# Optimization experiments

Measured on AMD Instinct MI355X. Metric: run time of the kernel, lower is better.

The kernel has to match this reference:

```python
import jax, jax.numpy as jnp
import numpy as np

B, S, D, H = 2, 2048, 1024, 16
HD = D // H  # head_dim = 64


def setup_inputs() -> dict:
    key = jax.random.key(0)
    ks = jax.random.split(key, 5)
    scale = 0.02
    return {
        "x": jax.random.normal(ks[0], (B, S, D), dtype=jnp.float32),
        "w_qkv": jax.random.normal(ks[1], (D, 3 * D), dtype=jnp.float32) * scale,
        "b_qkv": jax.random.normal(ks[2], (3 * D,), dtype=jnp.float32) * scale,
        "w_out": jax.random.normal(ks[3], (D, D), dtype=jnp.float32) * scale,
        "b_out": jax.random.normal(ks[4], (D,), dtype=jnp.float32) * scale,
    }


def reference(x, w_qkv, b_qkv, w_out, b_out):
    b, s, d = x.shape
    qkv = x @ w_qkv + b_qkv                       # [b,s,3d]
    q, k, v = jnp.split(qkv, 3, axis=-1)
    # split heads -> [b,h,s,hd]
    def split_heads(t):
        return t.reshape(b, s, H, HD).transpose(0, 2, 1, 3)
    q, k, v = split_heads(q), split_heads(k), split_heads(v)
    scores = jnp.einsum('bhqd,bhkd->bhqk', q, k) / jnp.sqrt(jnp.float32(HD))
    causal = jnp.tril(jnp.ones((s, s), dtype=bool))  # [s,s]
    scores = jnp.where(causal[None, None], scores, -jnp.inf)
    attn = jax.nn.softmax(scores, axis=-1)        # dropout_p=0 -> identity
    ctx = jnp.einsum('bhqk,bhkd->bhqd', attn, v)
    ctx = ctx.transpose(0, 2, 1, 3).reshape(b, s, d)  # merge heads
    return ctx @ w_out + b_out
```

## Files before the change

### kernel.cpp

```cpp
#include <hip/hip_runtime.h>
#include <hip/hip_bf16.h>

#define B_ 2
#define S_ 2048
#define D_ 1024
#define H_ 16
#define HD_ 64
#define KDIM 1024
#define QKVW 3072

typedef __attribute__((ext_vector_type(8))) short s16x8;
typedef __attribute__((ext_vector_type(8))) __bf16 bf16x8;
typedef __attribute__((ext_vector_type(4))) float f32x4;
typedef __attribute__((ext_vector_type(16))) float f32x16;
typedef __attribute__((ext_vector_type(4))) unsigned short u16x4;

__device__ __forceinline__ unsigned short f2bf(float f) {
  union { __bf16 b; unsigned short u; } v;
  v.b = (__bf16)f;
  return v.u;
}

__device__ __forceinline__ unsigned pk2(float lo, float hi) {
  union { unsigned short s[2]; unsigned u; } r;
  r.s[0] = f2bf(lo); r.s[1] = f2bf(hi);
  return r.u;
}

__device__ __forceinline__ void plswap2(unsigned& a_out, unsigned& b_out,
                                        unsigned a, unsigned b) {
  auto rr = __builtin_amdgcn_permlane32_swap(a, b, false, false);
  unsigned out[2];
  __builtin_memcpy(out, &rr, 8);
  a_out = out[0];
  b_out = out[1];
}

#define MFMA16(a, b, c) __builtin_amdgcn_mfma_f32_16x16x32_bf16((a), (b), (c), 0, 0, 0)
#define MFMA32(a, b, c) __builtin_amdgcn_mfma_f32_32x32x16_bf16((a), (b), (c), 0, 0, 0)

__device__ __forceinline__ void gll16(const void* g, void* l) {
  __builtin_amdgcn_global_load_lds(
      (const __attribute__((address_space(1))) void*)g,
      (__attribute__((address_space(3))) void*)l, 16, 0, 0);
}

__global__ __launch_bounds__(256) void prep(const float* __restrict__ X,
                                            unsigned short* __restrict__ Xb,
                                            const float* __restrict__ Wq,
                                            unsigned short* __restrict__ WqT,
                                            const float* __restrict__ Wo,
                                            unsigned short* __restrict__ WoT) {
  const int bid = blockIdx.x;
  const int t = threadIdx.x;
  if (bid < 2048) {
    const int i = (bid * 256 + t) * 8;
    const float4 a = *reinterpret_cast<const float4*>(X + i);
    const float4 b = *reinterpret_cast<const float4*>(X + i + 4);
    u16x4 lo = {f2bf(a.x), f2bf(a.y), f2bf(a.z), f2bf(a.w)};
    u16x4 hi = {f2bf(b.x), f2bf(b.y), f2bf(b.z), f2bf(b.w)};
    *reinterpret_cast<u16x4*>(Xb + i) = lo;
    *reinterpret_cast<u16x4*>(Xb + i + 4) = hi;
    return;
  }
  __shared__ float T[64][65];
  const float* W;
  unsigned short* Wt;
  int N, k0, n0;
  if (bid < 2048 + 768) {
    const int i = bid - 2048;
    W = Wq; Wt = WqT; N = 3072;
    n0 = (i % 48) * 64; k0 = (i / 48) * 64;
  } else {
    const int i = bid - 2816;
    W = Wo; Wt = WoT; N = 1024;
    n0 = (i % 16) * 64; k0 = (i / 16) * 64;
  }
  const int lr = t >> 4, lc = (t & 15) * 4;
#pragma unroll
  for (int p = 0; p < 4; ++p) {
    const int r = lr + p * 16;
    const float4 v = *reinterpret_cast<const float4*>(W + (size_t)(k0 + r) * N + n0 + lc);
    T[r][lc + 0] = v.x; T[r][lc + 1] = v.y; T[r][lc + 2] = v.z; T[r][lc + 3] = v.w;
  }
  __syncthreads();
  const int wn = t >> 4, wk = (t & 15) * 4;
#pragma unroll
  for (int p = 0; p < 4; ++p) {
    const int n = wn + p * 16;
    u16x4 o = {f2bf(T[wk + 0][n]), f2bf(T[wk + 1][n]), f2bf(T[wk + 2][n]), f2bf(T[wk + 3][n])};
    *reinterpret_cast<u16x4*>(Wt + (size_t)(n0 + n) * 1024 + k0 + wk) = o;
  }
}

__global__ __launch_bounds__(256) void vtrans(const unsigned short* __restrict__ QKVc,
                                              unsigned short* __restrict__ Vt) {
  __shared__ unsigned short T[64][72];
  const int s0 = blockIdx.x * 64;
  const int bh = blockIdx.y;
  const int bb = bh >> 4, hh = bh & 15;
  const int t = threadIdx.x;
  const size_t base = (size_t)bh * (S_ * HD_);
  const int r = t >> 3, c8 = (t & 7) * 8;
#pragma unroll
  for (int p = 0; p < 2; ++p)
    *reinterpret_cast<s16x8*>(&T[r + p * 32][c8]) =
        *reinterpret_cast<const s16x8*>(
            QKVc + (size_t)(bb * S_ + s0 + r + p * 32) * QKVW + 2048 + hh * 64 + c8);
  __syncthreads();
  const int hd = t & 63, sg = (t >> 6) * 8;
#pragma unroll
  for (int p = 0; p < 2; ++p) {
    unsigned short tmp[8];
#pragma unroll
    for (int j = 0; j < 8; ++j) tmp[j] = T[sg + p * 32 + j][hd];
    *reinterpret_cast<s16x8*>(Vt + base + (size_t)hd * S_ + s0 + sg + p * 32) =
        *reinterpret_cast<s16x8*>(tmp);
  }
}

__global__ __launch_bounds__(256) void gemm_qkv(
    const unsigned short* __restrict__ Xb, const unsigned short* __restrict__ WT,
    const float* __restrict__ bias, unsigned short* __restrict__ Cq) {
  __shared__ __align__(16) unsigned short As[2][64 * 64];
  __shared__ __align__(16) unsigned short Bs[2][128 * 64];
  const int bid = blockIdx.y * 24 + blockIdx.x;
  const int xcd = bid & 7, rr = bid >> 3;
  const int m0 = ((xcd >> 1) * 16 + (rr & 15)) * 64;
  const int n0 = ((xcd & 1) * 12 + (rr >> 4)) * 128;
  const int t = threadIdx.x;
  const int lane = t & 63, wid = t >> 6;
  const int wr = wid >> 1, wc = wid & 1;
  const int l15 = lane & 15, l16 = lane >> 4;
  const int srow = lane >> 3, scol = ((lane & 7) ^ srow) << 3;
  f32x4 acc[2][4] = {};

#define GSTAGE(buf, k0)                                                              \
  do {                                                                               \
    _Pragma("unroll") for (int c = 0; c < 2; ++c) {                                  \
      const int r8 = wid * 16 + c * 8;                                               \
      gll16(Xb + (size_t)(m0 + r8 + srow) * KDIM + (k0) + scol, &As[buf][r8 * 64]);  \
    }                                                                                \
    _Pragma("unroll") for (int c = 0; c < 4; ++c) {                                  \
      const int r8 = wid * 32 + c * 8;                                               \
      gll16(WT + (size_t)(n0 + r8 + srow) * KDIM + (k0) + scol, &Bs[buf][r8 * 64]);  \
    }                                                                                \
  } while (0)

  GSTAGE(0, 0);
  for (int kt = 0; kt < 16; ++kt) {
    const int cur = kt & 1;
    if (kt + 1 < 16) {
      GSTAGE(cur ^ 1, (kt + 1) * 64);
      __asm__ volatile("s_waitcnt vmcnt(6)" ::: "memory");
    } else {
      __asm__ volatile("s_waitcnt vmcnt(0)" ::: "memory");
    }
    __builtin_amdgcn_s_barrier();
    const int key = (l15 & 7) << 4;
    const char* ab = (const char*)&As[cur][0] + (wr * 32 + l15) * 128;
    const char* bb = (const char*)&Bs[cur][0] + (wc * 64 + l15) * 128;
#pragma unroll
    for (int ks = 0; ks < 2; ++ks) {
      bf16x8 af[2], bfr[4];
#pragma unroll
      for (int m = 0; m < 2; ++m)
        af[m] = *(const bf16x8*)(ab + m * 2048 + ((ks * 64 + l16 * 16) ^ key));
#pragma unroll
      for (int n = 0; n < 4; ++n)
        bfr[n] = *(const bf16x8*)(bb + n * 2048 + ((ks * 64 + l16 * 16) ^ key));
#pragma unroll
      for (int m = 0; m < 2; ++m)
#pragma unroll
        for (int n = 0; n < 4; ++n)
          acc[m][n] = MFMA16(af[m], bfr[n], acc[m][n]);
    }
    __builtin_amdgcn_s_barrier();
  }
#pragma unroll
  for (int n = 0; n < 4; ++n) {
    const int col = n0 + wc * 64 + n * 16 + l15;
    const float bv = bias[col];
#pragma unroll
    for (int m = 0; m < 2; ++m) {
#pragma unroll
      for (int j = 0; j < 4; ++j) {
        const int row = m0 + wr * 32 + m * 16 + l16 * 4 + j;
        Cq[(size_t)row * QKVW + col] = f2bf(acc[m][n][j] + bv);
      }
    }
  }
}

__global__ __launch_bounds__(256, 3) void attn(
    const unsigned short* __restrict__ QKVc, const unsigned short* __restrict__ Vt,
    unsigned short* __restrict__ Cxt) {
  __shared__ __align__(16) unsigned short Kl[2][2][4096];
  __shared__ __align__(16) unsigned short Vl[2][4096];
  const int bi = blockIdx.x;
  const int xcd = bi & 7, slot = bi >> 3;
  const int bh = xcd * 4 + (slot & 3);
  const int qt = 31 - (slot >> 2);
  const int t = threadIdx.x, lane = t & 63, wid = t >> 6;
  const int qw = wid & 1, pw = wid >> 1;
  const int l31 = lane & 31, h = lane >> 5;
  const int h8 = h * 8, h16 = h * 16, h4 = h * 4;
  const int bb = bh >> 4, hh = bh & 15;
  const size_t base = (size_t)bh * (S_ * HD_);
  const int q0 = qt * 64 + qw * 32;
  const float NEG = -1e30f;
  const float SCALE = 0.18033688011112042f;
  const float FM = 10.0f;
  const int srow = lane >> 3;
  const int scol = ((lane & 7) ^ srow) << 3;

  bf16x8 qf[4];
  {
    const unsigned short* qp =
        QKVc + (size_t)(bb * S_ + q0 + l31) * QKVW + hh * 64 + h8;
#pragma unroll
    for (int ks = 0; ks < 4; ++ks) qf[ks] = *reinterpret_cast<const bf16x8*>(qp + ks * 16);
  }
  f32x16 o0 = {}, o1 = {};
  float lacc[8] = {};

#define STAGEK(buf, kvb)                                                              \
  do {                                                                                \
    _Pragma("unroll") for (int c = 0; c < 8; ++c)                                     \
      gll16(QKVc + (size_t)(bb * S_ + (kvb) + c * 8 + srow) * QKVW + 1024 +           \
                hh * 64 + scol,                                                       \
            &Kl[buf][pw][c * 8 * 64]);                                                \
  } while (0)

#define STAGEV(kvb)                                                                   \
  do {                                                                                \
    _Pragma("unroll") for (int c = 0; c < 8; ++c)                                     \
      gll16(Vt + base + (size_t)(c * 8 + srow) * S_ + (kvb) + scol,                   \
            &Vl[pw][c * 8 * 64]);                                                     \
  } while (0)

#define COMPUTE_QK(cb, tcur)                                                         \
  do {                                                                               \
    const int kv0 = (tcur) * 64;                                                     \
    const bool diag = (kv0 + 63 > q0);                                               \
    const char* kbase = (const char*)&Kl[cb][pw][0];                                 \
    const int key = (l31 & 7) << 4;                                                  \
    f32x16 s0 = {}, s1 = {};                                                         \
    __builtin_amdgcn_s_setprio(1);                                                   \
    _Pragma("unroll") for (int ks = 0; ks < 4; ++ks) {                               \
      bf16x8 ka = *(const bf16x8*)(kbase + l31 * 128 + ((ks * 32 + h16) ^ key));     \
      s0 = MFMA32(ka, qf[ks], s0);                                                   \
    }                                                                                \
    if (f2) {                                                                        \
      _Pragma("unroll") for (int ks = 0; ks < 4; ++ks) {                             \
        bf16x8 kb = *(const bf16x8*)(kbase + (32 + l31) * 128 + ((ks * 32 + h16) ^ key)); \
        s1 = MFMA32(kb, qf[ks], s1);                                                 \
      }                                                                              \
    }                                                                                \
    __builtin_amdgcn_s_setprio(0);                                                   \
    if (diag) {                                                                      \
      const int lim0 = q0 + l31 - kv0;                                               \
      const int lim1 = lim0 - 32;                                                    \
      _Pragma("unroll") for (int r = 0; r < 16; ++r) {                               \
        const int cr = (r & 3) + 8 * (r >> 2) + h4;                                  \
        if (cr > lim0) s0[r] = NEG;                                                  \
        if (f2 && cr > lim1) s1[r] = NEG;                                            \
      }                                                                              \
    }                                                                                \
    _Pragma("unroll") for (int r = 0; r < 16; ++r)                                   \
      s0[r] = exp2f(fmaf(s0[r], SCALE, -FM));                                        \
    if (f2) {                                                                        \
      _Pragma("unroll") for (int r = 0; r < 16; ++r)                                 \
        s1[r] = exp2f(fmaf(s1[r], SCALE, -FM));                                      \
    }                                                                                \
    _Pragma("unroll") for (int r = 0; r < 8; ++r) {                                  \
      float ps = s0[r] + s0[r + 8];                                                  \
      if (f2) ps += s1[r] + s1[r + 8];                                               \
      lacc[r] += ps;                                                                 \
    }                                                                                \
    {                                                                                \
      union { unsigned u[4]; bf16x8 v; } uu;                                         \
      unsigned a0, a1, a2, a3, w0, w1, w2, w3;                                       \
      w0 = pk2(s0[0], s0[1]); w1 = pk2(s0[2], s0[3]);                                \
      w2 = pk2(s0[4], s0[5]); w3 = pk2(s0[6], s0[7]);                                \
      plswap2(a0, a2, w0, w2); plswap2(a1, a3, w1, w3);                              \
      uu.u[0] = a0; uu.u[1] = a1; uu.u[2] = a2; uu.u[3] = a3; pa[0] = uu.v;          \
      w0 = pk2(s0[8], s0[9]); w1 = pk2(s0[10], s0[11]);                              \
      w2 = pk2(s0[12], s0[13]); w3 = pk2(s0[14], s0[15]);                            \
      plswap2(a0, a2, w0, w2); plswap2(a1, a3, w1, w3);                              \
      uu.u[0] = a0; uu.u[1] = a1; uu.u[2] = a2; uu.u[3] = a3; pa[1] = uu.v;          \
      if (f2) {                                                                      \
        w0 = pk2(s1[0], s1[1]); w1 = pk2(s1[2], s1[3]);                              \
        w2 = pk2(s1[4], s1[5]); w3 = pk2(s1[6], s1[7]);                              \
        plswap2(a0, a2, w0, w2); plswap2(a1, a3, w1, w3);                            \
        uu.u[0] = a0; uu.u[1] = a1; uu.u[2] = a2; uu.u[3] = a3; pa[2] = uu.v;        \
        w0 = pk2(s1[8], s1[9]); w1 = pk2(s1[10], s1[11]);                            \
        w2 = pk2(s1[12], s1[13]); w3 = pk2(s1[14], s1[15]);                          \
        plswap2(a0, a2, w0, w2); plswap2(a1, a3, w1, w3);                            \
        uu.u[0] = a0; uu.u[1] = a1; uu.u[2] = a2; uu.u[3] = a3; pa[3] = uu.v;        \
      }                                                                              \
    }                                                                                \
  } while (0)

#define COMPUTE_PV()                                                                 \
  do {                                                                               \
    const char* vbase = (const char*)&Vl[pw][0];                                     \
    const int key = (l31 & 7) << 4;                                                  \
    __builtin_amdgcn_s_setprio(1);                                                   \
    _Pragma("unroll") for (int hb = 0; hb < 2; ++hb) {                               \
      _Pragma("unroll") for (int ks = 0; ks < 4; ++ks)                               \
        if (f2 || ks < 2) {                                                          \
          bf16x8 va = *(const bf16x8*)(vbase + (hb * 32 + l31) * 128 +               \
                                       ((ks * 32 + h16) ^ key));                     \
          if (hb == 0) o0 = MFMA32(va, pa[ks], o0);                                  \
          else         o1 = MFMA32(va, pa[ks], o1);                                  \
        }                                                                            \
    }                                                                                \
    __builtin_amdgcn_s_setprio(0);                                                   \
  } while (0)

  const int npair = (qt >> 1) + 1;
  if (qw == 0 && pw <= qt) STAGEK(0, pw * 64);
  for (int p = 0; p < npair; ++p) {
    const int cb = p & 1;
    const int tcur = 2 * p + pw;
    if (qw == 1 && tcur <= qt) STAGEV(tcur * 64);
    if (qw == 0) {
      if (tcur + 2 <= qt) {
        STAGEK(cb ^ 1, (tcur + 2) * 64);
        __asm__ volatile("s_waitcnt vmcnt(8)" ::: "memory");
      } else {
        __asm__ volatile("s_waitcnt vmcnt(0)" ::: "memory");
      }
    }
    __builtin_amdgcn_s_barrier();
    bf16x8 pa[4];
    const bool f2 = (tcur * 64 + 32 <= q0 + 31);
    if (tcur <= qt) COMPUTE_QK(cb, tcur);
    if (qw == 1) __asm__ volatile("s_waitcnt vmcnt(0)" ::: "memory");
    __builtin_amdgcn_s_barrier();
    if (tcur <= qt) COMPUTE_PV();
    __builtin_amdgcn_s_barrier();
  }

  float lrow = 0.f;
#pragma unroll
  for (int r = 0; r < 8; ++r) lrow += lacc[r];
  lrow += __shfl_xor(lrow, 32);

  float* mb = (float*)&Kl[0][0][0];
  const int mi = qw * 2112 + lane * 33;
  if (pw == 1) {
#pragma unroll
    for (int r = 0; r < 16; ++r) { mb[mi + r] = o0[r]; mb[mi + 16 + r] = o1[r]; }
    mb[mi + 32] = lrow;
  }
  __syncthreads();
  if (pw == 1) return;
#pragma unroll
  for (int r = 0; r < 16; ++r) { o0[r] += mb[mi + r]; o1[r] += mb[mi + 16 + r]; }
  lrow += mb[mi + 32];

  float* obuf = (float*)&Vl[0][0] + (size_t)qw * 2048;
  const float rl = 1.0f / lrow;
#pragma unroll
  for (int r = 0; r < 16; ++r) {
    const int cr = (r & 3) + 8 * (r >> 2) + h4;
    obuf[l31 * 64 + (cr ^ ((l31 & 7) << 2))] = o0[r] * rl;
    obuf[l31 * 64 + ((32 + cr) ^ ((l31 & 7) << 2))] = o1[r] * rl;
  }
  __asm__ volatile("s_waitcnt lgkmcnt(0)" ::: "memory");
#pragma unroll
  for (int p = 0; p < 8; ++p) {
    const int r = (lane >> 4) + p * 4;
    const int ce = ((lane & 15) * 4) ^ ((r & 7) << 2);
    const f32x4 v = *reinterpret_cast<const f32x4*>(&obuf[r * 64 + ce]);
    u16x4 wv = {f2bf(v[0]), f2bf(v[1]), f2bf(v[2]), f2bf(v[3])};
    *reinterpret_cast<u16x4*>(&Cxt[base + (size_t)(q0 + r) * HD_ + (lane & 15) * 4]) = wv;
  }
}

__global__ __launch_bounds__(256) void gemm_out(
    const unsigned short* __restrict__ Cxt, const unsigned short* __restrict__ WT,
    const float* __restrict__ bias, float* __restrict__ out) {
  constexpr int NM = 1024;
  __shared__ __align__(16) unsigned short As[2][64 * 64];
  __shared__ __align__(16) unsigned short Bs[2][128 * 64];
  const int bid = blockIdx.y * 8 + blockIdx.x;
  const int xcd = bid & 7, rr = bid >> 3;
  const int m0 = ((xcd >> 1) * 16 + (rr & 15)) * 64;
  const int n0 = ((xcd & 1) * 4 + (rr >> 4)) * 128;
  const int t = threadIdx.x;
  const int lane = t & 63, wid = t >> 6;
  const int wr = wid >> 1, wc = wid & 1;
  const int l15 = lane & 15, l16 = lane >> 4;
  const int srow = lane >> 3, scol = ((lane & 7) ^ srow) << 3;
  f32x4 acc[2][4] = {};

#define OSTAGE(buf, k0)                                                              \
  do {                                                                               \
    const int head = (k0) >> 6;                                                      \
    _Pragma("unroll") for (int c = 0; c < 2; ++c) {                                  \
      const int r8 = wid * 16 + c * 8;                                               \
      const int gr = m0 + r8 + srow;                                                 \
      gll16(Cxt + ((((size_t)(gr >> 11) * H_ + head) << 11) + (gr & 2047)) * HD_ + scol, \
            &As[buf][r8 * 64]);                                                      \
    }                                                                                \
    _Pragma("unroll") for (int c = 0; c < 4; ++c) {                                  \
      const int r8 = wid * 32 + c * 8;                                               \
      gll16(WT + (size_t)(n0 + r8 + srow) * KDIM + (k0) + scol, &Bs[buf][r8 * 64]);  \
    }                                                                                \
  } while (0)

  OSTAGE(0, 0);
  for (int kt = 0; kt < 16; ++kt) {
    const int cur = kt & 1;
    if (kt + 1 < 16) {
      OSTAGE(cur ^ 1, (kt + 1) * 64);
      __asm__ volatile("s_waitcnt vmcnt(6)" ::: "memory");
    } else {
      __asm__ volatile("s_waitcnt vmcnt(0)" ::: "memory");
    }
    __builtin_amdgcn_s_barrier();
    const int key = (l15 & 7) << 4;
    const char* ab = (const char*)&As[cur][0] + (wr * 32 + l15) * 128;
    const char* bb = (const char*)&Bs[cur][0] + (wc * 64 + l15) * 128;
#pragma unroll
    for (int ks = 0; ks < 2; ++ks) {
      bf16x8 af[2], bfr[4];
#pragma unroll
      for (int m = 0; m < 2; ++m)
        af[m] = *(const bf16x8*)(ab + m * 2048 + ((ks * 64 + l16 * 16) ^ key));
#pragma unroll
      for (int n = 0; n < 4; ++n)
        bfr[n] = *(const bf16x8*)(bb + n * 2048 + ((ks * 64 + l16 * 16) ^ key));
#pragma unroll
      for (int m = 0; m < 2; ++m)
#pragma unroll
        for (int n = 0; n < 4; ++n)
          acc[m][n] = MFMA16(af[m], bfr[n], acc[m][n]);
    }
    __builtin_amdgcn_s_barrier();
  }
#pragma unroll
  for (int n = 0; n < 4; ++n) {
    const int col = n0 + wc * 64 + n * 16 + l15;
    const float bv = bias[col];
#pragma unroll
    for (int m = 0; m < 2; ++m) {
#pragma unroll
      for (int j = 0; j < 4; ++j) {
        const int row = m0 + wr * 32 + m * 16 + l16 * 4 + j;
        out[(size_t)row * NM + col] = acc[m][n][j] + bv;
      }
    }
  }
}

extern "C" void kernel_launch(void* const* d_in, const int* in_sizes, int n_in,
                              void* d_out, int out_size, void* d_ws, size_t ws_size,
                              hipStream_t stream) {
  const float* x = (const float*)d_in[0];
  const float* w_qkv = (const float*)d_in[1];
  const float* b_qkv = (const float*)d_in[2];
  const float* w_out = (const float*)d_in[3];
  const float* b_out = (const float*)d_in[4];
  float* out = (float*)d_out;

  const size_t NTOK = (size_t)B_ * H_ * S_ * HD_;
  unsigned short* QKVc = (unsigned short*)d_ws;
  unsigned short* Vt = QKVc + (size_t)4096 * QKVW;
  unsigned short* WqT = Vt + NTOK;
  unsigned short* WoT = WqT + (size_t)3072 * 1024;
  unsigned short* Xbf = WoT + (size_t)1024 * 1024;
  unsigned short* Cxt = Xbf;

  hipLaunchKernelGGL(prep, dim3(2048 + 768 + 256), dim3(256), 0, stream,
                     x, Xbf, w_qkv, WqT, w_out, WoT);
  hipLaunchKernelGGL(gemm_qkv, dim3(24, 64), dim3(256), 0, stream, Xbf, WqT, b_qkv, QKVc);
  hipLaunchKernelGGL(vtrans, dim3(32, 32), dim3(256), 0, stream, QKVc, Vt);
  hipLaunchKernelGGL(attn, dim3(1024), dim3(256), 0, stream, QKVc, Vt, Cxt);
  hipLaunchKernelGGL(gemm_out, dim3(8, 64), dim3(256), 0, stream, Cxt, WoT, b_out, out);
}
```

Baseline: 106.4 us.

## Double attention query tile per block to reuse K/V tiles across two Q subtiles

```diff
diff --git a/kernel.cpp b/kernel.cpp
--- a/kernel.cpp
+++ b/kernel.cpp
@@ -192,7 +192,7 @@
   }
 }
 
-__global__ __launch_bounds__(256, 3) void attn(
+__global__ __launch_bounds__(256, 2) void attn(
     const unsigned short* __restrict__ QKVc, const unsigned short* __restrict__ Vt,
     unsigned short* __restrict__ Cxt) {
   __shared__ __align__(16) unsigned short Kl[2][2][4096];
@@ -200,29 +200,35 @@
   const int bi = blockIdx.x;
   const int xcd = bi & 7, slot = bi >> 3;
   const int bh = xcd * 4 + (slot & 3);
-  const int qt = 31 - (slot >> 2);
+  const int sq = slot >> 2;
+  const int qt = (slot < 32) ? (15 - sq) : (sq - 8);
   const int t = threadIdx.x, lane = t & 63, wid = t >> 6;
   const int qw = wid & 1, pw = wid >> 1;
   const int l31 = lane & 31, h = lane >> 5;
   const int h8 = h * 8, h16 = h * 16, h4 = h * 4;
   const int bb = bh >> 4, hh = bh & 15;
   const size_t base = (size_t)bh * (S_ * HD_);
-  const int q0 = qt * 64 + qw * 32;
+  const int q0 = qt * 128 + qw * 64;
+  const int tmax = 2 * qt + 1;
+  const int tdiag = 2 * qt + qw;
   const float NEG = -1e30f;
   const float SCALE = 0.18033688011112042f;
   const float FM = 10.0f;
   const int srow = lane >> 3;
   const int scol = ((lane & 7) ^ srow) << 3;
 
-  bf16x8 qf[4];
+  bf16x8 qfa[4], qfb[4];
   {
-    const unsigned short* qp =
-        QKVc + (size_t)(bb * S_ + q0 + l31) * QKVW + hh * 64 + h8;
-#pragma unroll
-    for (int ks = 0; ks < 4; ++ks) qf[ks] = *reinterpret_cast<const bf16x8*>(qp + ks * 16);
-  }
-  f32x16 o0 = {}, o1 = {};
-  float lacc[8] = {};
+    const unsigned short* qp = QKVc + (size_t)(bb * S_ + q0 + l31) * QKVW + hh * 64 + h8;
+    const unsigned short* qp2 = qp + (size_t)32 * QKVW;
+#pragma unroll
+    for (int ks = 0; ks < 4; ++ks) {
+      qfa[ks] = *reinterpret_cast<const bf16x8*>(qp + ks * 16);
+      qfb[ks] = *reinterpret_cast<const bf16x8*>(qp2 + ks * 16);
+    }
+  }
+  f32x16 oa0 = {}, oa1 = {}, ob0 = {}, ob1 = {};
+  float lacc_a[8] = {}, lacc_b[8] = {};
 
 #define STAGEK(buf, kvb)                                                              \
   do {                                                                                \
@@ -239,94 +245,38 @@
             &Vl[pw][c * 8 * 64]);                                                     \
   } while (0)
 
-#define COMPUTE_QK(cb, tcur)                                                         \
-  do {                                                                               \
-    const int kv0 = (tcur) * 64;                                                     \
-    const bool diag = (kv0 + 63 > q0);                                               \
-    const char* kbase = (const char*)&Kl[cb][pw][0];                                 \
-    const int key = (l31 & 7) << 4;                                                  \
-    f32x16 s0 = {}, s1 = {};                                                         \
-    __builtin_amdgcn_s_setprio(1);                                                   \
-    _Pragma("unroll") for (int ks = 0; ks < 4; ++ks) {                               \
-      bf16x8 ka = *(const bf16x8*)(kbase + l31 * 128 + ((ks * 32 + h16) ^ key));     \
-      s0 = MFMA32(ka, qf[ks], s0);                                                   \
-    }                                                                                \
-    if (f2) {                                                                        \
-      _Pragma("unroll") for (int ks = 0; ks < 4; ++ks) {                             \
-        bf16x8 kb = *(const bf16x8*)(kbase + (32 + l31) * 128 + ((ks * 32 + h16) ^ key)); \
-        s1 = MFMA32(kb, qf[ks], s1);                                                 \
-      }                                                                              \
-    }                                                                                \
-    __builtin_amdgcn_s_setprio(0);                                                   \
-    if (diag) {                                                                      \
-      const int lim0 = q0 + l31 - kv0;                                               \
-      const int lim1 = lim0 - 32;                                                    \
-      _Pragma("unroll") for (int r = 0; r < 16; ++r) {                               \
-        const int cr = (r & 3) + 8 * (r >> 2) + h4;                                  \
-        if (cr > lim0) s0[r] = NEG;                                                  \
-        if (f2 && cr > lim1) s1[r] = NEG;                                            \
-      }                                                                              \
-    }                                                                                \
-    _Pragma("unroll") for (int r = 0; r < 16; ++r)                                   \
-      s0[r] = exp2f(fmaf(s0[r], SCALE, -FM));                                        \
-    if (f2) {                                                                        \
-      _Pragma("unroll") for (int r = 0; r < 16; ++r)                                 \
-        s1[r] = exp2f(fmaf(s1[r], SCALE, -FM));                                      \
-    }                                                                                \
-    _Pragma("unroll") for (int r = 0; r < 8; ++r) {                                  \
-      float ps = s0[r] + s0[r + 8];                                                  \
-      if (f2) ps += s1[r] + s1[r + 8];                                               \
-      lacc[r] += ps;                                                                 \
-    }                                                                                \
-    {                                                                                \
-      union { unsigned u[4]; bf16x8 v; } uu;                                         \
-      unsigned a0, a1, a2, a3, w0, w1, w2, w3;                                       \
-      w0 = pk2(s0[0], s0[1]); w1 = pk2(s0[2], s0[3]);                                \
-      w2 = pk2(s0[4], s0[5]); w3 = pk2(s0[6], s0[7]);                                \
-      plswap2(a0, a2, w0, w2); plswap2(a1, a3, w1, w3);                              \
-      uu.u[0] = a0; uu.u[1] = a1; uu.u[2] = a2; uu.u[3] = a3; pa[0] = uu.v;          \
-      w0 = pk2(s0[8], s0[9]); w1 = pk2(s0[10], s0[11]);                              \
-      w2 = pk2(s0[12], s0[13]); w3 = pk2(s0[14], s0[15]);                            \
-      plswap2(a0, a2, w0, w2); plswap2(a1, a3, w1, w3);                              \
-      uu.u[0] = a0; uu.u[1] = a1; uu.u[2] = a2; uu.u[3] = a3; pa[1] = uu.v;          \
-      if (f2) {                                                                      \
-        w0 = pk2(s1[0], s1[1]); w1 = pk2(s1[2], s1[3]);                              \
-        w2 = pk2(s1[4], s1[5]); w3 = pk2(s1[6], s1[7]);                              \
-        plswap2(a0, a2, w0, w2); plswap2(a1, a3, w1, w3);                            \
-        uu.u[0] = a0; uu.u[1] = a1; uu.u[2] = a2; uu.u[3] = a3; pa[2] = uu.v;        \
-        w0 = pk2(s1[8], s1[9]); w1 = pk2(s1[10], s1[11]);                            \
-        w2 = pk2(s1[12], s1[13]); w3 = pk2(s1[14], s1[15]);                          \
-        plswap2(a0, a2, w0, w2); plswap2(a1, a3, w1, w3);                            \
-        uu.u[0] = a0; uu.u[1] = a1; uu.u[2] = a2; uu.u[3] = a3; pa[3] = uu.v;        \
-      }                                                                              \
-    }                                                                                \
+#define PACK(PD, S0, S1, two)                                                         \
+  do {                                                                                \
+    union { unsigned u[4]; bf16x8 v; } uu;                                            \
+    unsigned a0, a1, a2, a3, w0, w1, w2, w3;                                          \
+    w0 = pk2(S0[0], S0[1]); w1 = pk2(S0[2], S0[3]);                                   \
+    w2 = pk2(S0[4], S0[5]); w3 = pk2(S0[6], S0[7]);                                   \
+    plswap2(a0, a2, w0, w2); plswap2(a1, a3, w1, w3);                                 \
+    uu.u[0] = a0; uu.u[1] = a1; uu.u[2] = a2; uu.u[3] = a3; PD[0] = uu.v;             \
+    w0 = pk2(S0[8], S0[9]); w1 = pk2(S0[10], S0[11]);                                 \
+    w2 = pk2(S0[12], S0[13]); w3 = pk2(S0[14], S0[15]);                               \
+    plswap2(a0, a2, w0, w2); plswap2(a1, a3, w1, w3);                                 \
+    uu.u[0] = a0; uu.u[1] = a1; uu.u[2] = a2; uu.u[3] = a3; PD[1] = uu.v;             \
+    if (two) {                                                                        \
+      w0 = pk2(S1[0], S1[1]); w1 = pk2(S1[2], S1[3]);                                 \
+      w2 = pk2(S1[4], S1[5]); w3 = pk2(S1[6], S1[7]);                                 \
+      plswap2(a0, a2, w0, w2); plswap2(a1, a3, w1, w3);                               \
+      uu.u[0] = a0; uu.u[1] = a1; uu.u[2] = a2; uu.u[3] = a3; PD[2] = uu.v;           \
+      w0 = pk2(S1[8], S1[9]); w1 = pk2(S1[10], S1[11]);                               \
+      w2 = pk2(S1[12], S1[13]); w3 = pk2(S1[14], S1[15]);                             \
+      plswap2(a0, a2, w0, w2); plswap2(a1, a3, w1, w3);                               \
+      uu.u[0] = a0; uu.u[1] = a1; uu.u[2] = a2; uu.u[3] = a3; PD[3] = uu.v;           \
+    }                                                                                 \
   } while (0)
 
-#define COMPUTE_PV()                                                                 \
-  do {                                                                               \
-    const char* vbase = (const char*)&Vl[pw][0];                                     \
-    const int key = (l31 & 7) << 4;                                                  \
-    __builtin_amdgcn_s_setprio(1);                                                   \
-    _Pragma("unroll") for (int hb = 0; hb < 2; ++hb) {                               \
-      _Pragma("unroll") for (int ks = 0; ks < 4; ++ks)                               \
-        if (f2 || ks < 2) {                                                          \
-          bf16x8 va = *(const bf16x8*)(vbase + (hb * 32 + l31) * 128 +               \
-                                       ((ks * 32 + h16) ^ key));                     \
-          if (hb == 0) o0 = MFMA32(va, pa[ks], o0);                                  \
-          else         o1 = MFMA32(va, pa[ks], o1);                                  \
-        }                                                                            \
-    }                                                                                \
-    __builtin_amdgcn_s_setprio(0);                                                   \
-  } while (0)
-
-  const int npair = (qt >> 1) + 1;
-  if (qw == 0 && pw <= qt) STAGEK(0, pw * 64);
+  const int npair = qt + 1;
+  if (qw == 0) STAGEK(0, pw * 64);
   for (int p = 0; p < npair; ++p) {
     const int cb = p & 1;
     const int tcur = 2 * p + pw;
-    if (qw == 1 && tcur <= qt) STAGEV(tcur * 64);
+    if (qw == 1) STAGEV(tcur * 64);
     if (qw == 0) {
-      if (tcur + 2 <= qt) {
+      if (tcur + 2 <= tmax) {
         STAGEK(cb ^ 1, (tcur + 2) * 64);
         __asm__ volatile("s_waitcnt vmcnt(8)" ::: "memory");
       } else {
@@ -334,50 +284,130 @@
       }
     }
     __builtin_amdgcn_s_barrier();
-    bf16x8 pa[4];
-    const bool f2 = (tcur * 64 + 32 <= q0 + 31);
-    if (tcur <= qt) COMPUTE_QK(cb, tcur);
+    bf16x8 pa[4], pb[4];
+    const bool active = (tcur <= tdiag);
+    const bool diag = (tcur == tdiag);
+    if (active) {
+      const char* kbase = (const char*)&Kl[cb][pw][0];
+      const int key = (l31 & 7) << 4;
+      f32x16 sa0 = {}, sa1 = {}, sb0 = {}, sb1 = {};
+      __builtin_amdgcn_s_setprio(1);
+#pragma unroll
+      for (int ks = 0; ks < 4; ++ks) {
+        bf16x8 ka = *(const bf16x8*)(kbase + l31 * 128 + ((ks * 32 + h16) ^ key));
+        sa0 = MFMA32(ka, qfa[ks], sa0);
+        sb0 = MFMA32(ka, qfb[ks], sb0);
+      }
+      if (!diag) {
+#pragma unroll
+        for (int ks = 0; ks < 4; ++ks) {
+          bf16x8 kb = *(const bf16x8*)(kbase + (32 + l31) * 128 + ((ks * 32 + h16) ^ key));
+          sa1 = MFMA32(kb, qfa[ks], sa1);
+          sb1 = MFMA32(kb, qfb[ks], sb1);
+        }
+      } else {
+#pragma unroll
+        for (int ks = 0; ks < 4; ++ks) {
+          bf16x8 kb = *(const bf16x8*)(kbase + (32 + l31) * 128 + ((ks * 32 + h16) ^ key));
+          sb1 = MFMA32(kb, qfb[ks], sb1);
+        }
+      }
+      __builtin_amdgcn_s_setprio(0);
+      if (diag) {
+#pragma unroll
+        for (int r = 0; r < 16; ++r) {
+          const int cr = (r & 3) + 8 * (r >> 2) + h4;
+          if (cr > l31) { sa0[r] = NEG; sb1[r] = NEG; }
+        }
+      }
+#pragma unroll
+      for (int r = 0; r < 16; ++r) {
+        sa0[r] = exp2f(fmaf(sa0[r], SCALE, -FM));
+        sb0[r] = exp2f(fmaf(sb0[r], SCALE, -FM));
+        sb1[r] = exp2f(fmaf(sb1[r], SCALE, -FM));
+      }
+      if (!diag) {
+#pragma unroll
+        for (int r = 0; r < 16; ++r) sa1[r] = exp2f(fmaf(sa1[r], SCALE, -FM));
+      }
+#pragma unroll
+      for (int r = 0; r < 8; ++r) {
+        float psa = sa0[r] + sa0[r + 8];
+        if (!diag) psa += sa1[r] + sa1[r + 8];
+        lacc_a[r] += psa;
+        lacc_b[r] += (sb0[r] + sb0[r + 8]) + (sb1[r] + sb1[r + 8]);
+      }
+      PACK(pa, sa0, sa1, (!diag));
+      PACK(pb, sb0, sb1, true);
+    }
     if (qw == 1) __asm__ volatile("s_waitcnt vmcnt(0)" ::: "memory");
     __builtin_amdgcn_s_barrier();
-    if (tcur <= qt) COMPUTE_PV();
-    __builtin_amdgcn_s_barrier();
-  }
-
-  float lrow = 0.f;
-#pragma unroll
-  for (int r = 0; r < 8; ++r) lrow += lacc[r];
-  lrow += __shfl_xor(lrow, 32);
+    if (active) {
+      const char* vbase = (const char*)&Vl[pw][0];
+      const int key = (l31 & 7) << 4;
+      __builtin_amdgcn_s_setprio(1);
+#pragma unroll
+      for (int ks = 0; ks < 4; ++ks) {
+        bf16x8 v0 = *(const bf16x8*)(vbase + l31 * 128 + ((ks * 32 + h16) ^ key));
+        bf16x8 v1 = *(const bf16x8*)(vbase + (32 + l31) * 128 + ((ks * 32 + h16) ^ key));
+        if (ks < 2 || !diag) {
+          oa0 = MFMA32(v0, pa[ks], oa0);
+          oa1 = MFMA32(v1, pa[ks], oa1);
+        }
+        ob0 = MFMA32(v0, pb[ks], ob0);
+        ob1 = MFMA32(v1, pb[ks], ob1);
+      }
+      __builtin_amdgcn_s_setprio(0);
+    }
+    __builtin_amdgcn_s_barrier();
+  }
+
+  float lra = 0.f, lrb = 0.f;
+#pragma unroll
+  for (int r = 0; r < 8; ++r) { lra += lacc_a[r]; lrb += lacc_b[r]; }
+  lra += __shfl_xor(lra, 32);
+  lrb += __shfl_xor(lrb, 32);
 
   float* mb = (float*)&Kl[0][0][0];
-  const int mi = qw * 2112 + lane * 33;
-  if (pw == 1) {
-#pragma unroll
-    for (int r = 0; r < 16; ++r) { mb[mi + r] = o0[r]; mb[mi + 16 + r] = o1[r]; }
-    mb[mi + 32] = lrow;
-  }
+  float* obuf = (float*)&Vl[0][0] + qw * 2048;
+  const int mi = (qw * 64 + lane) * 33;
+
+#define MERGE_EPI(O0, O1, LR, q0h)                                                    \
+  do {                                                                                \
+    if (pw == 1) {                                                                    \
+      _Pragma("unroll") for (int r = 0; r < 16; ++r) {                                \
+        mb[mi + r] = O0[r]; mb[mi + 16 + r] = O1[r];                                  \
+      }                                                                               \
+      mb[mi + 32] = LR;                                                               \
+    }                                                                                 \
+    __syncthreads();                                                                  \
+    if (pw == 0) {                                                                    \
+      _Pragma("unroll") for (int r = 0; r < 16; ++r) {                                \
+        O0[r] += mb[mi + r]; O1[r] += mb[mi + 16 + r];                                \
+      }                                                                               \
+      const float lrt = LR + mb[mi + 32];                                             \
+      const float rl = 1.0f / lrt;                                                    \
+      _Pragma("unroll") for (int r = 0; r < 16; ++r) {                                \
+        const int cr = (r & 3) + 8 * (r >> 2) + h4;                                   \
+        obuf[l31 * 64 + (cr ^ ((l31 & 7) << 2))] = O0[r] * rl;                        \
+        obuf[l31 * 64 + ((32 + cr) ^ ((l31 & 7) << 2))] = O1[r] * rl;                 \
+      }                                                                               \
+      __asm__ volatile("s_waitcnt lgkmcnt(0)" ::: "memory");                          \
+      _Pragma("unroll") for (int p2 = 0; p2 < 8; ++p2) {                              \
+        const int r = (lane >> 4) + p2 * 4;                                           \
+        const int ce = ((lane & 15) * 4) ^ ((r & 7) << 2);                            \
+        const f32x4 v = *reinterpret_cast<const f32x4*>(&obuf[r * 64 + ce]);          \
+        u16x4 wv = {f2bf(v[0]), f2bf(v[1]), f2bf(v[2]), f2bf(v[3])};                  \
+        *reinterpret_cast<u16x4*>(                                                    \
+            &Cxt[base + (size_t)((q0h) + r) * HD_ + (lane & 15) * 4]) = wv;           \
+      }                                                                               \
+    }                                                                                 \
+    __syncthreads();                                                                  \
+  } while (0)
+
   __syncthreads();
-  if (pw == 1) return;
-#pragma unroll
-  for (int r = 0; r < 16; ++r) { o0[r] += mb[mi + r]; o1[r] += mb[mi + 16 + r]; }
-  lrow += mb[mi + 32];
-
-  float* obuf = (float*)&Vl[0][0] + (size_t)qw * 2048;
-  const float rl = 1.0f / lrow;
-#pragma unroll
-  for (int r = 0; r < 16; ++r) {
-    const int cr = (r & 3) + 8 * (r >> 2) + h4;
-    obuf[l31 * 64 + (cr ^ ((l31 & 7) << 2))] = o0[r] * rl;
-    obuf[l31 * 64 + ((32 + cr) ^ ((l31 & 7) << 2))] = o1[r] * rl;
-  }
-  __asm__ volatile("s_waitcnt lgkmcnt(0)" ::: "memory");
-#pragma unroll
-  for (int p = 0; p < 8; ++p) {
-    const int r = (lane >> 4) + p * 4;
-    const int ce = ((lane & 15) * 4) ^ ((r & 7) << 2);
-    const f32x4 v = *reinterpret_cast<const f32x4*>(&obuf[r * 64 + ce]);
-    u16x4 wv = {f2bf(v[0]), f2bf(v[1]), f2bf(v[2]), f2bf(v[3])};
-    *reinterpret_cast<u16x4*>(&Cxt[base + (size_t)(q0 + r) * HD_ + (lane & 15) * 4]) = wv;
-  }
+  MERGE_EPI(oa0, oa1, lra, q0);
+  MERGE_EPI(ob0, ob1, lrb, q0 + 32);
 }
 
 __global__ __launch_bounds__(256) void gemm_out(
@@ -479,6 +509,6 @@
                      x, Xbf, w_qkv, WqT, w_out, WoT);
   hipLaunchKernelGGL(gemm_qkv, dim3(24, 64), dim3(256), 0, stream, Xbf, WqT, b_qkv, QKVc);
   hipLaunchKernelGGL(vtrans, dim3(32, 32), dim3(256), 0, stream, QKVc, Vt);
-  hipLaunchKernelGGL(attn, dim3(1024), dim3(256), 0, stream, QKVc, Vt, Cxt);
+  hipLaunchKernelGGL(attn, dim3(512), dim3(256), 0, stream, QKVc, Vt, Cxt);
   hipLaunchKernelGGL(gemm_out, dim3(8, 64), dim3(256), 0, stream, Cxt, WoT, b_out, out);
 }
```

Measured after the change: 111.0 us. +4.2%, slower.
